# Optimization experiments

Measured on AMD Instinct MI355X. Metric: run time of the kernel, lower is better.

## Reference

```python
import jax, jax.numpy as jnp
import numpy as np

H = 4096      # hidden_size
NH = 32       # num heads
HD = H // NH  # head_dim = 128
I = 11008     # intermediate_size
T = 2048      # num tokens (single prompt sequence)
G = 128       # AWQ group size
EPS = 1e-6
ROPE_BASE = 10000.0


def _make_qlinear(key, k_in, n_out):
    k1, k2, k3 = jax.random.split(key, 3)
    qw = jax.random.randint(k1, (k_in, n_out), 0, 16, dtype=jnp.int32)
    qz = jax.random.randint(k2, (k_in // G, n_out), 0, 16, dtype=jnp.int32)
    scales = jax.random.uniform(k3, (k_in // G, n_out), dtype=jnp.float32) * 0.01 + 1e-3
    return qw, scales, qz


def setup_inputs() -> dict:
    key = jax.random.key(0)
    ks = jax.random.split(key, 8)
    inp = {
        "positions": jnp.arange(T, dtype=jnp.int64),
        "hidden_states": jax.random.normal(ks[0], (T, H), dtype=jnp.float32),
        "input_ln_w": jnp.ones((H,), dtype=jnp.float32),
        "post_ln_w": jnp.ones((H,), dtype=jnp.float32),
    }
    inp["qkv_qw"], inp["qkv_scales"], inp["qkv_qz"] = _make_qlinear(ks[1], H, 3 * H)
    inp["o_qw"], inp["o_scales"], inp["o_qz"] = _make_qlinear(ks[2], H, H)
    inp["gu_qw"], inp["gu_scales"], inp["gu_qz"] = _make_qlinear(ks[3], H, 2 * I)
    inp["down_qw"], inp["down_scales"], inp["down_qz"] = _make_qlinear(ks[4], I, H)
    return inp


def rms_norm(x, w):
    var = jnp.mean(x * x, axis=-1, keepdims=True)
    return x * jax.lax.rsqrt(var + EPS) * w


def awq_linear(x, qw, scales, qz):
    # dequant: (q - z) * scale, group-wise along K; then dense GEMM
    w = (qw.astype(scales.dtype) - jnp.repeat(qz.astype(scales.dtype), G, axis=0)) \
        * jnp.repeat(scales, G, axis=0)
    return x @ w


def apply_rope(x, positions):
    # x: [T, NH, HD], neox-style half rotation, rotary_dim = HD
    inv_freq = 1.0 / (ROPE_BASE ** (jnp.arange(0, HD, 2, dtype=jnp.float32) / HD))
    ang = positions.astype(jnp.float32)[:, None] * inv_freq  # [T, HD/2]
    cos = jnp.cos(ang)[:, None, :]
    sin = jnp.sin(ang)[:, None, :]
    x1, x2 = x[..., : HD // 2], x[..., HD // 2:]
    return jnp.concatenate([x1 * cos - x2 * sin, x2 * cos + x1 * sin], axis=-1)


def reference(positions, hidden_states, input_ln_w, post_ln_w,
              qkv_qw, qkv_scales, qkv_qz, o_qw, o_scales, o_qz,
              gu_qw, gu_scales, gu_qz, down_qw, down_scales, down_qz):
    residual = hidden_states
    x = rms_norm(hidden_states, input_ln_w)

    # attention
    qkv = awq_linear(x, qkv_qw, qkv_scales, qkv_qz)  # [T, 3H]
    q, k, v = jnp.split(qkv, 3, axis=-1)
    q = apply_rope(q.reshape(T, NH, HD), positions)
    k = apply_rope(k.reshape(T, NH, HD), positions)
    v = v.reshape(T, NH, HD)
    scale = HD ** -0.5
    scores = jnp.einsum('qhd,khd->hqk', q, k) * scale  # [NH, T, T]
    causal = jnp.tril(jnp.ones((T, T), dtype=bool))
    scores = jnp.where(causal[None], scores, jnp.finfo(scores.dtype).min)
    probs = jax.nn.softmax(scores, axis=-1)
    attn = jnp.einsum('hqk,khd->qhd', probs, v).reshape(T, H)
    attn_out = awq_linear(attn, o_qw, o_scales, o_qz)

    hidden = residual + attn_out
    residual = hidden
    x = rms_norm(hidden, post_ln_w)

    # MLP: gate_up -> silu(gate) * up -> down
    gate_up = awq_linear(x, gu_qw, gu_scales, gu_qz)  # [T, 2I]
    gate, up = jnp.split(gate_up, 2, axis=-1)
    x = jax.nn.silu(gate) * up
    x = awq_linear(x, down_qw, down_scales, down_qz)
    return residual + x
```

## Files before the change

### kernel.cpp

```cpp
#include <hip/hip_runtime.h>
#include <stdint.h>

#define T_SEQ 2048
#define HID 4096
#define NHEADS 32
#define I_FF 11008
#define QKV_N 12288
#define GU_N 22016

typedef unsigned short u16;
typedef unsigned int u32;
typedef __attribute__((ext_vector_type(4))) float f32x4;
typedef __attribute__((ext_vector_type(8))) __bf16 bf16x8;
typedef __attribute__((ext_vector_type(4))) u32 u32x4;
typedef __attribute__((ext_vector_type(2))) u32 u32x2;

__device__ __forceinline__ u16 f2bf(float f) {
  union { float f; u32 u; } v; v.f = f;
  u32 u = v.u;
  return (u16)((u + 0x7fffu + ((u >> 16) & 1u)) >> 16);
}
__device__ __forceinline__ float bf2f(u16 h) {
  union { u32 u; float f; } v; v.u = ((u32)h) << 16;
  return v.f;
}
__device__ __forceinline__ void split2(float x, u16& hi, u16& lo) {
  hi = f2bf(x);
  lo = f2bf(x - bf2f(hi));
}
__device__ __forceinline__ void split8(const float* v, u32x4& H, u32x4& L) {
#pragma unroll
  for (int j = 0; j < 4; j++) {
    u16 h0, l0, h1, l1;
    split2(v[2 * j], h0, l0);
    split2(v[2 * j + 1], h1, l1);
    H[j] = (u32)h0 | ((u32)h1 << 16);
    L[j] = (u32)l0 | ((u32)l1 << 16);
  }
}
__device__ __forceinline__ void dq8(u32 rbp, int zq, u32x4& w) {
#pragma unroll
  for (int j = 0; j < 4; j++) {
    int q0 = (int)((rbp >> (8 * j)) & 15u) - zq;
    int q1 = (int)((rbp >> (8 * j + 4)) & 15u) - zq;
    u32 b0 = __builtin_bit_cast(u32, (float)q0);
    u32 b1 = __builtin_bit_cast(u32, (float)q1);
    w[j] = (b0 >> 16) | (b1 & 0xffff0000u);
  }
}

__global__ __launch_bounds__(256) void pack_qw_kernel(
    const int* __restrict__ qw, u32* __restrict__ pw, int N) {
  int n = blockIdx.x * 256 + threadIdx.x;
  int oct = blockIdx.y;
  const int* src = qw + (size_t)oct * 8 * N + n;
  u32 v = 0;
#pragma unroll
  for (int j = 0; j < 8; j++)
    v |= ((u32)src[(size_t)j * N] & 15u) << (4 * j);
  pw[(size_t)oct * N + n] = v;
}

__global__ __launch_bounds__(256) void rmsnorm_kernel(
    const float* __restrict__ in, const float* __restrict__ w,
    u16* __restrict__ outh, u16* __restrict__ outl) {
  int row = blockIdx.x;
  const float* x = in + (size_t)row * HID;
  float4 vals[4];
  float ss = 0.f;
#pragma unroll
  for (int k = 0; k < 4; k++) {
    vals[k] = ((const float4*)x)[threadIdx.x + k * 256];
    ss += vals[k].x * vals[k].x + vals[k].y * vals[k].y +
          vals[k].z * vals[k].z + vals[k].w * vals[k].w;
  }
#pragma unroll
  for (int o = 1; o < 64; o <<= 1) ss += __shfl_xor(ss, o);
  __shared__ float red[4];
  if ((threadIdx.x & 63) == 0) red[threadIdx.x >> 6] = ss;
  __syncthreads();
  ss = red[0] + red[1] + red[2] + red[3];
  float rs = rsqrtf(ss * (1.f / HID) + 1e-6f);
#pragma unroll
  for (int k = 0; k < 4; k++) {
    int c4 = threadIdx.x + k * 256;
    float4 wv = ((const float4*)w)[c4];
    float o[4] = {vals[k].x * rs * wv.x, vals[k].y * rs * wv.y,
                  vals[k].z * rs * wv.z, vals[k].w * rs * wv.w};
    u32x2 H, L;
#pragma unroll
    for (int j = 0; j < 2; j++) {
      u16 h0, l0, h1, l1;
      split2(o[2 * j], h0, l0);
      split2(o[2 * j + 1], h1, l1);
      H[j] = (u32)h0 | ((u32)h1 << 16);
      L[j] = (u32)l0 | ((u32)l1 << 16);
    }
    *(u32x2*)(outh + (size_t)row * HID + c4 * 4) = H;
    *(u32x2*)(outl + (size_t)row * HID + c4 * 4) = L;
  }
}

template <bool RESID, bool OUTBF16>
__global__ __launch_bounds__(512) void awq_gemm_kernel(
    const u16* __restrict__ Ahg, const u16* __restrict__ Alg,
    const u32* __restrict__ pw, const float* __restrict__ scales,
    const int* __restrict__ qz, const float* __restrict__ resid,
    void* __restrict__ outp, int N, int K, int nstrips) {
  __shared__ u16 AhL[2][128][40];
  __shared__ u16 AlL[2][128][40];
  __shared__ u16 BqL[2][128][40];
  int tid = threadIdx.x;
  int lane = tid & 63;
  int wid = tid >> 6;
  int g16 = lane >> 4, l16 = lane & 15;
  int p = blockIdx.x;
  int xcd = p & 7;
  int idx = p >> 3;
  int s = idx >> 1;
  int mi = ((idx & 1) << 3) + xcd;
  if (s >= nstrips) return;
  int m0 = mi * 128;
  int n0 = s * 128;
  int wr = wid >> 1, wc = wid & 1;

  f32x4 acc[2][4] = {};
  float svold[4];

  int a_row = tid >> 2, a_kc = (tid & 3) * 8;
  const u16* aph = Ahg + (size_t)(m0 + a_row) * K + a_kc;
  const u16* apl = Alg + (size_t)(m0 + a_row) * K + a_kc;
  int b_n = tid & 127, b_kb = (tid >> 7) * 8;
  const u32* pwp = pw + (size_t)(tid >> 7) * N + n0 + b_n;
  const float* scp = scales + n0;
  const int* qzp = qz + n0 + b_n;

  int nsteps = K >> 5;

  u32x4 rah, ral;
  u32 rbp;

  auto load_step = [&](int ks) {
    int k0 = ks << 5;
    rah = *(const u32x4*)(aph + k0);
    ral = *(const u32x4*)(apl + k0);
    rbp = pwp[(size_t)(ks << 2) * N];
  };
  auto write_step = [&](int buf, int zq) {
    *(u32x4*)&AhL[buf][a_row][a_kc] = rah;
    *(u32x4*)&AlL[buf][a_row][a_kc] = ral;
    u32x4 w;
    dq8(rbp, zq, w);
    *(u32x4*)&BqL[buf][b_n][b_kb] = w;
  };

  int zq = qzp[0];
  load_step(0);
  write_step(0, zq);
#pragma unroll
  for (int n = 0; n < 4; n++)
    svold[n] = scp[wc * 64 + n * 16 + l16];
  __syncthreads();

  int cur = 0;
  for (int ks = 0; ks < nsteps; ks++) {
    int nxt = ks + 1;
    if (nxt < nsteps) {
      if ((nxt & 3) == 0) zq = qzp[(size_t)(nxt >> 2) * N];
      load_step(nxt);
    }
    if (ks != 0 && (ks & 3) == 0) {
      int g = ks >> 2;
#pragma unroll
      for (int n = 0; n < 4; n++) {
        float svnew = scp[(size_t)g * N + wc * 64 + n * 16 + l16];
        float r = svold[n] * __builtin_amdgcn_rcpf(svnew);
        svold[n] = svnew;
#pragma unroll
        for (int m = 0; m < 2; m++)
#pragma unroll
          for (int i = 0; i < 4; i++) acc[m][n][i] *= r;
      }
    }
    bf16x8 bq[4];
#pragma unroll
    for (int n = 0; n < 4; n++)
      bq[n] = __builtin_bit_cast(bf16x8,
          *(const u32x4*)&BqL[cur][wc * 64 + n * 16 + l16][g16 * 8]);
#pragma unroll
    for (int m = 0; m < 2; m++) {
      bf16x8 ah = __builtin_bit_cast(bf16x8,
          *(const u32x4*)&AhL[cur][wr * 32 + m * 16 + l16][g16 * 8]);
      bf16x8 al = __builtin_bit_cast(bf16x8,
          *(const u32x4*)&AlL[cur][wr * 32 + m * 16 + l16][g16 * 8]);
#pragma unroll
      for (int n = 0; n < 4; n++) {
        acc[m][n] = __builtin_amdgcn_mfma_f32_16x16x32_bf16(al, bq[n], acc[m][n], 0, 0, 0);
        acc[m][n] = __builtin_amdgcn_mfma_f32_16x16x32_bf16(ah, bq[n], acc[m][n], 0, 0, 0);
      }
    }
    if (nxt < nsteps) write_step(cur ^ 1, zq);
    __syncthreads();
    cur ^= 1;
  }
#pragma unroll
  for (int n = 0; n < 4; n++)
#pragma unroll
    for (int m = 0; m < 2; m++)
#pragma unroll
      for (int i = 0; i < 4; i++) acc[m][n][i] *= svold[n];
#pragma unroll
  for (int m = 0; m < 2; m++) {
#pragma unroll
    for (int n = 0; n < 4; n++) {
#pragma unroll
      for (int r = 0; r < 4; r++) {
        int row = m0 + wr * 32 + m * 16 + g16 * 4 + r;
        int col = n0 + wc * 64 + n * 16 + l16;
        float v = acc[m][n][r];
        if (RESID) v += resid[(size_t)row * N + col];
        if (OUTBF16)
          ((u16*)outp)[(size_t)row * N + col] = f2bf(v);
        else
          ((float*)outp)[(size_t)row * N + col] = v;
      }
    }
  }
}

template <bool RESID, bool OUTBF16>
__global__ __launch_bounds__(512) void awq_gemm256_kernel(
    const u16* __restrict__ Ahg,
    const u32* __restrict__ pw, const float* __restrict__ scales,
    const int* __restrict__ qz, const float* __restrict__ resid,
    void* __restrict__ outp, int N, int K, int nstrips) {
  __shared__ u16 AhL[2][128][40];
  __shared__ u16 BqL[2][256][40];
  int tid = threadIdx.x;
  int lane = tid & 63;
  int wid = tid >> 6;
  int g16 = lane >> 4, l16 = lane & 15;
  int p = blockIdx.x;
  int xcd = p & 7;
  int idx = p >> 3;
  int s = idx >> 1;
  int mi = ((idx & 1) << 3) + xcd;
  if (s >= nstrips) return;
  int m0 = mi * 128;
  int n0 = s * 256;
  int wr = wid >> 2, wc = wid & 3;

  f32x4 acc[4][4] = {};
  float svold[4];

  int a_row = tid >> 2, a_kc = (tid & 3) * 8;
  const u16* aph = Ahg + (size_t)(m0 + a_row) * K + a_kc;
  int b_n = tid & 255;
  int b_oct = (tid >> 8) * 2;
  int b_kb = b_oct * 8;
  const u32* pwp = pw + (size_t)b_oct * N + n0 + b_n;
  const float* scp = scales + n0;
  const int* qzp = qz + n0 + b_n;

  int nsteps = K >> 5;

  u32x4 rah;
  u32 rb0, rb1;

  auto load_step = [&](int ks) {
    int k0 = ks << 5;
    rah = *(const u32x4*)(aph + k0);
    const u32* q = pwp + (size_t)(ks << 2) * N;
    rb0 = q[0];
    rb1 = q[N];
  };
  auto write_step = [&](int buf, int zq) {
    *(u32x4*)&AhL[buf][a_row][a_kc] = rah;
    u32x4 w0, w1;
    dq8(rb0, zq, w0);
    dq8(rb1, zq, w1);
    *(u32x4*)&BqL[buf][b_n][b_kb] = w0;
    *(u32x4*)&BqL[buf][b_n][b_kb + 8] = w1;
  };

  int zq = qzp[0];
  load_step(0);
  write_step(0, zq);
#pragma unroll
  for (int n = 0; n < 4; n++)
    svold[n] = scp[wc * 64 + n * 16 + l16];
  __syncthreads();

  int cur = 0;
  for (int ks = 0; ks < nsteps; ks++) {
    int nxt = ks + 1;
    if (nxt < nsteps) {
      if ((nxt & 3) == 0) zq = qzp[(size_t)(nxt >> 2) * N];
      load_step(nxt);
    }
    if (ks != 0 && (ks & 3) == 0) {
      int g = ks >> 2;
#pragma unroll
      for (int n = 0; n < 4; n++) {
        float svnew = scp[(size_t)g * N + wc * 64 + n * 16 + l16];
        float r = svold[n] * __builtin_amdgcn_rcpf(svnew);
        svold[n] = svnew;
#pragma unroll
        for (int m = 0; m < 4; m++)
#pragma unroll
          for (int i = 0; i < 4; i++) acc[m][n][i] *= r;
      }
    }
    bf16x8 bq[4];
#pragma unroll
    for (int n = 0; n < 4; n++)
      bq[n] = __builtin_bit_cast(bf16x8,
          *(const u32x4*)&BqL[cur][wc * 64 + n * 16 + l16][g16 * 8]);
#pragma unroll
    for (int m = 0; m < 4; m++) {
      bf16x8 ah = __builtin_bit_cast(bf16x8,
          *(const u32x4*)&AhL[cur][wr * 64 + m * 16 + l16][g16 * 8]);
#pragma unroll
      for (int n = 0; n < 4; n++)
        acc[m][n] = __builtin_amdgcn_mfma_f32_16x16x32_bf16(ah, bq[n], acc[m][n], 0, 0, 0);
    }
    if (nxt < nsteps) write_step(cur ^ 1, zq);
    __syncthreads();
    cur ^= 1;
  }
#pragma unroll
  for (int n = 0; n < 4; n++)
#pragma unroll
    for (int m = 0; m < 4; m++)
#pragma unroll
      for (int i = 0; i < 4; i++) acc[m][n][i] *= svold[n];
#pragma unroll
  for (int m = 0; m < 4; m++) {
#pragma unroll
    for (int n = 0; n < 4; n++) {
#pragma unroll
      for (int r = 0; r < 4; r++) {
        int row = m0 + wr * 64 + m * 16 + g16 * 4 + r;
        int col = n0 + wc * 64 + n * 16 + l16;
        float v = acc[m][n][r];
        if (RESID) v += resid[(size_t)row * N + col];
        if (OUTBF16)
          ((u16*)outp)[(size_t)row * N + col] = f2bf(v);
        else
          ((float*)outp)[(size_t)row * N + col] = v;
      }
    }
  }
}

__global__ __launch_bounds__(256) void rope_kernel(float* __restrict__ qkv) {
  int t = blockIdx.x;
  __shared__ float cs[64], sn[64];
  if (threadIdx.x < 64) {
    int i = threadIdx.x;
    float freq = exp2f(-(float)i * (13.287712379549449f / 64.f));
    float ang = (float)t * freq;
    cs[i] = cosf(ang);
    sn[i] = sinf(ang);
  }
  __syncthreads();
#pragma unroll
  for (int it = 0; it < 16; it++) {
    int idx = threadIdx.x + it * 256;
    int part = idx >> 11;
    int rem = idx & 2047;
    int hh = rem >> 6, i = rem & 63;
    float* base = qkv + (size_t)t * QKV_N + (size_t)part * HID + hh * 128;
    float x1 = base[i], x2 = base[64 + i];
    float c = cs[i], s = sn[i];
    base[i] = x1 * c - x2 * s;
    base[64 + i] = x2 * c + x1 * s;
  }
}

__global__ __launch_bounds__(256) void transpose_v_kernel(
    const float* __restrict__ qkv, u16* __restrict__ vt) {
  __shared__ u16 tile[64][65];
  int tb = blockIdx.x;
  int cb = blockIdx.y;
  int tid = threadIdx.x;
  int r = tid >> 2, c16 = (tid & 3) * 16;
  const float* src = qkv + (size_t)(tb * 64 + r) * QKV_N + 2 * HID + cb * 64 + c16;
  float v[16];
  *(float4*)&v[0] = *(const float4*)(src);
  *(float4*)&v[4] = *(const float4*)(src + 4);
  *(float4*)&v[8] = *(const float4*)(src + 8);
  *(float4*)&v[12] = *(const float4*)(src + 12);
#pragma unroll
  for (int i = 0; i < 16; i++) tile[r][c16 + i] = f2bf(v[i]);
  __syncthreads();
  int ocol = tid >> 2, tchunk = (tid & 3) * 16;
  u16 vbuf[16];
#pragma unroll
  for (int i = 0; i < 16; i++) vbuf[i] = tile[tchunk + i][ocol];
  u16* dst = vt + (size_t)(cb * 64 + ocol) * T_SEQ + tb * 64 + tchunk;
  *(u32x4*)dst = *(u32x4*)&vbuf[0];
  *(u32x4*)(dst + 8) = *(u32x4*)&vbuf[8];
}

__global__ __launch_bounds__(256) void attn_kernel(
    const float* __restrict__ qkv, const u16* __restrict__ vt,
    u16* __restrict__ outh, u16* __restrict__ outl) {
  constexpr float SCALE = 0.08838834764831845f;
  __shared__ u16 Kh[32][136], Kl[32][136];
  __shared__ u16 Vt_lds[128][40];
  __shared__ u16 P_lds[4][16][40];
  int tid = threadIdx.x;
  int wid = tid >> 6, lane = tid & 63;
  int g16 = lane >> 4, l16 = lane & 15;
  int h = blockIdx.x & 31;
  int qt = blockIdx.x >> 5;
  int qb = qt * 64;

  bf16x8 qh[4], ql[4];
  {
    const float* qsrc = qkv + (size_t)(qb + wid * 16 + l16) * QKV_N + h * 128;
#pragma unroll
    for (int ds = 0; ds < 4; ds++) {
      float v[8];
      *(float4*)&v[0] = *(const float4*)(qsrc + ds * 32 + g16 * 8);
      *(float4*)&v[4] = *(const float4*)(qsrc + ds * 32 + g16 * 8 + 4);
      u32x4 H, L;
      split8(v, H, L);
      qh[ds] = __builtin_bit_cast(bf16x8, H);
      ql[ds] = __builtin_bit_cast(bf16x8, L);
    }
  }
  f32x4 oacc[8] = {};
  float mrun[4] = {-1e30f, -1e30f, -1e30f, -1e30f};
  float lrun[4] = {0.f, 0.f, 0.f, 0.f};

  int st_k = tid >> 3, st_d = (tid & 7) * 16;
  int sv_d = tid >> 1, sv_k = (tid & 1) * 16;

  int ktiles = (qb + 64) >> 5;
  for (int kt = 0; kt < ktiles; kt++) {
    __syncthreads();
    {
      const float* src = qkv + (size_t)(kt * 32 + st_k) * QKV_N + HID + h * 128 + st_d;
      float v[16];
      *(float4*)&v[0] = *(const float4*)(src);
      *(float4*)&v[4] = *(const float4*)(src + 4);
      *(float4*)&v[8] = *(const float4*)(src + 8);
      *(float4*)&v[12] = *(const float4*)(src + 12);
      u32x4 H, L;
      split8(&v[0], H, L);
      *(u32x4*)&Kh[st_k][st_d] = H;
      *(u32x4*)&Kl[st_k][st_d] = L;
      split8(&v[8], H, L);
      *(u32x4*)&Kh[st_k][st_d + 8] = H;
      *(u32x4*)&Kl[st_k][st_d + 8] = L;
    }
    {
      const u16* src = vt + (size_t)(h * 128 + sv_d) * T_SEQ + kt * 32 + sv_k;
      *(u32x4*)&Vt_lds[sv_d][sv_k] = *(const u32x4*)src;
      *(u32x4*)&Vt_lds[sv_d][sv_k + 8] = *(const u32x4*)(src + 8);
    }
    __syncthreads();
    f32x4 sacc[2] = {};
#pragma unroll
    for (int kb = 0; kb < 2; kb++)
#pragma unroll
      for (int ds = 0; ds < 4; ds++) {
        bf16x8 kfh = __builtin_bit_cast(bf16x8,
            *(const u32x4*)&Kh[kb * 16 + l16][ds * 32 + g16 * 8]);
        bf16x8 kfl = __builtin_bit_cast(bf16x8,
            *(const u32x4*)&Kl[kb * 16 + l16][ds * 32 + g16 * 8]);
        sacc[kb] = __builtin_amdgcn_mfma_f32_16x16x32_bf16(qh[ds], kfh, sacc[kb], 0, 0, 0);
        sacc[kb] = __builtin_amdgcn_mfma_f32_16x16x32_bf16(ql[ds], kfh, sacc[kb], 0, 0, 0);
        sacc[kb] = __builtin_amdgcn_mfma_f32_16x16x32_bf16(qh[ds], kfl, sacc[kb], 0, 0, 0);
      }
    float p0v[4], p1v[4];
#pragma unroll
    for (int r = 0; r < 4; r++) {
      int qrow = qb + wid * 16 + g16 * 4 + r;
      bool msk0 = (kt * 32 + l16) > qrow;
      bool msk1 = (kt * 32 + 16 + l16) > qrow;
      float s0 = msk0 ? -1e30f : sacc[0][r] * SCALE;
      float s1 = msk1 ? -1e30f : sacc[1][r] * SCALE;
      float tm = fmaxf(s0, s1);
      tm = fmaxf(tm, __shfl_xor(tm, 1));
      tm = fmaxf(tm, __shfl_xor(tm, 2));
      tm = fmaxf(tm, __shfl_xor(tm, 4));
      tm = fmaxf(tm, __shfl_xor(tm, 8));
      float mnew = fmaxf(mrun[r], tm);
      float fac = __expf(mrun[r] - mnew);
      float p0 = msk0 ? 0.f : __expf(s0 - mnew);
      float p1 = msk1 ? 0.f : __expf(s1 - mnew);
      float ts = p0 + p1;
      ts += __shfl_xor(ts, 1);
      ts += __shfl_xor(ts, 2);
      ts += __shfl_xor(ts, 4);
      ts += __shfl_xor(ts, 8);
      lrun[r] = lrun[r] * fac + ts;
      mrun[r] = mnew;
      p0v[r] = p0; p1v[r] = p1;
#pragma unroll
      for (int db = 0; db < 8; db++) oacc[db][r] *= fac;
    }
#pragma unroll
    for (int r = 0; r < 4; r++) {
      P_lds[wid][g16 * 4 + r][l16] = f2bf(p0v[r]);
      P_lds[wid][g16 * 4 + r][16 + l16] = f2bf(p1v[r]);
    }
    __syncthreads();
    bf16x8 pa = __builtin_bit_cast(bf16x8, *(const u32x4*)&P_lds[wid][l16][g16 * 8]);
#pragma unroll
    for (int db = 0; db < 8; db++) {
      bf16x8 vb = __builtin_bit_cast(bf16x8,
          *(const u32x4*)&Vt_lds[db * 16 + l16][g16 * 8]);
      oacc[db] = __builtin_amdgcn_mfma_f32_16x16x32_bf16(pa, vb, oacc[db], 0, 0, 0);
    }
  }
#pragma unroll
  for (int r = 0; r < 4; r++) {
    int qrow = qb + wid * 16 + g16 * 4 + r;
    float inv = 1.f / lrun[r];
#pragma unroll
    for (int db = 0; db < 8; db++) {
      float v = oacc[db][r] * inv;
      u16 h16, l16v;
      split2(v, h16, l16v);
      size_t idx = (size_t)qrow * HID + h * 128 + db * 16 + l16;
      outh[idx] = h16;
      outl[idx] = l16v;
    }
  }
}

__global__ __launch_bounds__(256) void silu_mul_kernel(
    const u16* __restrict__ gu, u16* __restrict__ acth) {
  size_t e = ((size_t)blockIdx.x * 256 + threadIdx.x) * 8;
  size_t row = e / I_FF;
  int col = (int)(e % I_FF);
  const u16* gp = gu + row * GU_N + col;
  u32x4 gv = *(const u32x4*)gp;
  u32x4 uv = *(const u32x4*)(gp + I_FF);
  u32x4 H;
#pragma unroll
  for (int j = 0; j < 4; j++) {
    float g0 = bf2f((u16)(gv[j] & 0xffff)), g1 = bf2f((u16)(gv[j] >> 16));
    float u0 = bf2f((u16)(uv[j] & 0xffff)), u1 = bf2f((u16)(uv[j] >> 16));
    float o0 = g0 / (1.f + __expf(-g0)) * u0;
    float o1 = g1 / (1.f + __expf(-g1)) * u1;
    H[j] = (u32)f2bf(o0) | ((u32)f2bf(o1) << 16);
  }
  *(u32x4*)(acth + row * I_FF + col) = H;
}

extern "C" void kernel_launch(void* const* d_in, const int* in_sizes, int n_in,
                              void* d_out, int out_size, void* d_ws, size_t ws_size,
                              hipStream_t stream) {
  const float* hs    = (const float*)d_in[1];
  const float* ln1   = (const float*)d_in[2];
  const float* ln2   = (const float*)d_in[3];
  const int* qkv_qw  = (const int*)d_in[4];
  const float* qkv_s = (const float*)d_in[5];
  const int* qkv_z   = (const int*)d_in[6];
  const int* o_qw    = (const int*)d_in[7];
  const float* o_s   = (const float*)d_in[8];
  const int* o_z     = (const int*)d_in[9];
  const int* gu_qw   = (const int*)d_in[10];
  const float* gu_s  = (const float*)d_in[11];
  const int* gu_z    = (const int*)d_in[12];
  const int* dn_qw   = (const int*)d_in[13];
  const float* dn_s  = (const float*)d_in[14];
  const int* dn_z    = (const int*)d_in[15];

  char* ws = (char*)d_ws;
  u16*   xnh    = (u16*)(ws);
  u16*   xnl    = (u16*)(ws + (size_t)16777216);
  float* qkv    = (float*)(ws + (size_t)33554432);
  u16*   vt     = (u16*)(ws + (size_t)134217728);
  float* hidden = (float*)(ws + (size_t)150994944);
  u16*   gup    = (u16*)(ws + (size_t)184549376);
  u16*   attnh  = xnh;
  u16*   attnl  = xnl;
  u16*   acth   = (u16*)qkv;
  u32* pk_gup = (u32*)gup;
  u32* pk_qkv = (u32*)((char*)qkv + (size_t)50331648);

  auto grid128 = [](int N) { return 16 * (N / 128); };
  auto grid256 = [](int N) { return 16 * (N / 256); };

  rmsnorm_kernel<<<T_SEQ, 256, 0, stream>>>(hs, ln1, xnh, xnl);
  pack_qw_kernel<<<dim3(QKV_N / 256, HID / 8), 256, 0, stream>>>(qkv_qw, pk_gup, QKV_N);
  awq_gemm_kernel<false, false><<<grid128(QKV_N), 512, 0, stream>>>(
      xnh, xnl, pk_gup, qkv_s, qkv_z, nullptr, qkv, QKV_N, HID, QKV_N / 128);
  rope_kernel<<<T_SEQ, 256, 0, stream>>>(qkv);
  transpose_v_kernel<<<dim3(T_SEQ / 64, HID / 64), 256, 0, stream>>>(qkv, vt);
  attn_kernel<<<NHEADS * (T_SEQ / 64), 256, 0, stream>>>(qkv, vt, attnh, attnl);
  pack_qw_kernel<<<dim3(HID / 256, HID / 8), 256, 0, stream>>>(o_qw, pk_gup, HID);
  awq_gemm256_kernel<true, false><<<grid256(HID), 512, 0, stream>>>(
      attnh, pk_gup, o_s, o_z, hs, hidden, HID, HID, HID / 256);
  rmsnorm_kernel<<<T_SEQ, 256, 0, stream>>>(hidden, ln2, xnh, xnl);
  pack_qw_kernel<<<dim3(GU_N / 256, HID / 8), 256, 0, stream>>>(gu_qw, pk_qkv, GU_N);
  awq_gemm256_kernel<false, true><<<grid256(GU_N), 512, 0, stream>>>(
      xnh, pk_qkv, gu_s, gu_z, nullptr, gup, GU_N, HID, GU_N / 256);
  silu_mul_kernel<<<(T_SEQ * (size_t)I_FF / 8 / 256), 256, 0, stream>>>(gup, acth);
  pack_qw_kernel<<<dim3(HID / 256, I_FF / 8), 256, 0, stream>>>(dn_qw, pk_gup, HID);
  awq_gemm256_kernel<true, false><<<grid256(HID), 512, 0, stream>>>(
      acth, pk_gup, dn_s, dn_z, hidden, (float*)d_out, HID, I_FF, HID / 256);
}
```

Measured before the change: 1.804 ms.

## Pre-dequantize AWQ weights to N-major bf16 before the 256-wide GEMMs

Adds a pack kernel that subtracts zero points and converts the int4 weights to bf16, stored N-major with K contiguous. The o-proj, gate/up and down GEMMs then copy bf16 tiles straight into LDS with 16-byte loads instead of unpacking nibbles and dequantizing in the inner loop. Gate/up is split into two half launches so the bf16 weight buffer fits in the workspace. The trade is about four times more weight bytes written and read through global memory, in exchange for less ALU work and simpler shared-memory staging inside the GEMM.

```diff
diff --git a/kernel.cpp b/kernel.cpp
--- a/kernel.cpp
+++ b/kernel.cpp
@@ -59,6 +59,27 @@
   for (int j = 0; j < 8; j++)
     v |= ((u32)src[(size_t)j * N] & 15u) << (4 * j);
   pw[(size_t)oct * N + n] = v;
+}
+
+__global__ __launch_bounds__(256) void pack_dqb_kernel(
+    const int* __restrict__ qw, const int* __restrict__ qz,
+    u16* __restrict__ bw, int N, int K, int n_base) {
+  int nl = blockIdx.x * 256 + threadIdx.x;
+  int n = n_base + nl;
+  int k0 = blockIdx.y * 32;
+  int zq = qz[(size_t)(k0 >> 7) * N + n];
+  u16 row[32];
+#pragma unroll
+  for (int j = 0; j < 32; j++) {
+    int q = qw[(size_t)(k0 + j) * N + n];
+    u32 b = __builtin_bit_cast(u32, (float)(q - zq));
+    row[j] = (u16)(b >> 16);
+  }
+  u16* dst = bw + (size_t)nl * K + k0;
+  *(u32x4*)dst = *(u32x4*)&row[0];
+  *(u32x4*)(dst + 8) = *(u32x4*)&row[8];
+  *(u32x4*)(dst + 16) = *(u32x4*)&row[16];
+  *(u32x4*)(dst + 24) = *(u32x4*)&row[24];
 }
 
 __global__ __launch_bounds__(256) void rmsnorm_kernel(
@@ -229,11 +250,10 @@
 }
 
 template <bool RESID, bool OUTBF16>
-__global__ __launch_bounds__(512) void awq_gemm256_kernel(
-    const u16* __restrict__ Ahg,
-    const u32* __restrict__ pw, const float* __restrict__ scales,
-    const int* __restrict__ qz, const float* __restrict__ resid,
-    void* __restrict__ outp, int N, int K, int nstrips) {
+__global__ __launch_bounds__(512) void awq_gemm256b_kernel(
+    const u16* __restrict__ Ahg, const u16* __restrict__ bw,
+    const float* __restrict__ scales, const float* __restrict__ resid,
+    void* __restrict__ outp, int N, int K, int nstrips, int n_base) {
   __shared__ u16 AhL[2][128][40];
   __shared__ u16 BqL[2][256][40];
   int tid = threadIdx.x;
@@ -247,7 +267,8 @@
   int mi = ((idx & 1) << 3) + xcd;
   if (s >= nstrips) return;
   int m0 = mi * 128;
-  int n0 = s * 256;
+  int n0l = s * 256;
+  int n0 = n_base + n0l;
   int wr = wid >> 2, wc = wid & 3;
 
   f32x4 acc[4][4] = {};
@@ -255,37 +276,28 @@
 
   int a_row = tid >> 2, a_kc = (tid & 3) * 8;
   const u16* aph = Ahg + (size_t)(m0 + a_row) * K + a_kc;
-  int b_n = tid & 255;
-  int b_oct = (tid >> 8) * 2;
-  int b_kb = b_oct * 8;
-  const u32* pwp = pw + (size_t)b_oct * N + n0 + b_n;
+  int b_row = tid >> 1, b_kc = (tid & 1) * 16;
+  const u16* bwp = bw + (size_t)(n0l + b_row) * K + b_kc;
   const float* scp = scales + n0;
-  const int* qzp = qz + n0 + b_n;
 
   int nsteps = K >> 5;
 
-  u32x4 rah;
-  u32 rb0, rb1;
+  u32x4 rah, rb0, rb1;
 
   auto load_step = [&](int ks) {
     int k0 = ks << 5;
     rah = *(const u32x4*)(aph + k0);
-    const u32* q = pwp + (size_t)(ks << 2) * N;
-    rb0 = q[0];
-    rb1 = q[N];
+    rb0 = *(const u32x4*)(bwp + k0);
+    rb1 = *(const u32x4*)(bwp + k0 + 8);
   };
-  auto write_step = [&](int buf, int zq) {
+  auto write_step = [&](int buf) {
     *(u32x4*)&AhL[buf][a_row][a_kc] = rah;
-    u32x4 w0, w1;
-    dq8(rb0, zq, w0);
-    dq8(rb1, zq, w1);
-    *(u32x4*)&BqL[buf][b_n][b_kb] = w0;
-    *(u32x4*)&BqL[buf][b_n][b_kb + 8] = w1;
+    *(u32x4*)&BqL[buf][b_row][b_kc] = rb0;
+    *(u32x4*)&BqL[buf][b_row][b_kc + 8] = rb1;
   };
 
-  int zq = qzp[0];
   load_step(0);
-  write_step(0, zq);
+  write_step(0);
 #pragma unroll
   for (int n = 0; n < 4; n++)
     svold[n] = scp[wc * 64 + n * 16 + l16];
@@ -294,10 +306,7 @@
   int cur = 0;
   for (int ks = 0; ks < nsteps; ks++) {
     int nxt = ks + 1;
-    if (nxt < nsteps) {
-      if ((nxt & 3) == 0) zq = qzp[(size_t)(nxt >> 2) * N];
-      load_step(nxt);
-    }
+    if (nxt < nsteps) load_step(nxt);
     if (ks != 0 && (ks & 3) == 0) {
       int g = ks >> 2;
 #pragma unroll
@@ -324,7 +333,7 @@
       for (int n = 0; n < 4; n++)
         acc[m][n] = __builtin_amdgcn_mfma_f32_16x16x32_bf16(ah, bq[n], acc[m][n], 0, 0, 0);
     }
-    if (nxt < nsteps) write_step(cur ^ 1, zq);
+    if (nxt < nsteps) write_step(cur ^ 1);
     __syncthreads();
     cur ^= 1;
   }
@@ -582,28 +591,41 @@
   u16*   attnh  = xnh;
   u16*   attnl  = xnl;
   u16*   acth   = (u16*)qkv;
-  u32* pk_gup = (u32*)gup;
-  u32* pk_qkv = (u32*)((char*)qkv + (size_t)50331648);
+  u32* pk_nib  = (u32*)gup;
+  u16* bw_gup  = (u16*)gup;
+  u16* bw_qkv  = (u16*)qkv;
 
   auto grid128 = [](int N) { return 16 * (N / 128); };
-  auto grid256 = [](int N) { return 16 * (N / 256); };
+  auto grid256 = [](int ncols) { return 16 * (ncols / 256); };
 
   rmsnorm_kernel<<<T_SEQ, 256, 0, stream>>>(hs, ln1, xnh, xnl);
-  pack_qw_kernel<<<dim3(QKV_N / 256, HID / 8), 256, 0, stream>>>(qkv_qw, pk_gup, QKV_N);
+  pack_qw_kernel<<<dim3(QKV_N / 256, HID / 8), 256, 0, stream>>>(qkv_qw, pk_nib, QKV_N);
   awq_gemm_kernel<false, false><<<grid128(QKV_N), 512, 0, stream>>>(
-      xnh, xnl, pk_gup, qkv_s, qkv_z, nullptr, qkv, QKV_N, HID, QKV_N / 128);
+      xnh, xnl, pk_nib, qkv_s, qkv_z, nullptr, qkv, QKV_N, HID, QKV_N / 128);
   rope_kernel<<<T_SEQ, 256, 0, stream>>>(qkv);
   transpose_v_kernel<<<dim3(T_SEQ / 64, HID / 64), 256, 0, stream>>>(qkv, vt);
   attn_kernel<<<NHEADS * (T_SEQ / 64), 256, 0, stream>>>(qkv, vt, attnh, attnl);
-  pack_qw_kernel<<<dim3(HID / 256, HID / 8), 256, 0, stream>>>(o_qw, pk_gup, HID);
-  awq_gemm256_kernel<true, false><<<grid256(HID), 512, 0, stream>>>(
-      attnh, pk_gup, o_s, o_z, hs, hidden, HID, HID, HID / 256);
+
+  pack_dqb_kernel<<<dim3(HID / 256, HID / 32), 256, 0, stream>>>(
+      o_qw, o_z, bw_gup, HID, HID, 0);
+  awq_gemm256b_kernel<true, false><<<grid256(HID), 512, 0, stream>>>(
+      attnh, bw_gup, o_s, hs, hidden, HID, HID, HID / 256, 0);
+
   rmsnorm_kernel<<<T_SEQ, 256, 0, stream>>>(hidden, ln2, xnh, xnl);
-  pack_qw_kernel<<<dim3(GU_N / 256, HID / 8), 256, 0, stream>>>(gu_qw, pk_qkv, GU_N);
-  awq_gemm256_kernel<false, true><<<grid256(GU_N), 512, 0, stream>>>(
-      xnh, pk_qkv, gu_s, gu_z, nullptr, gup, GU_N, HID, GU_N / 256);
+
+  pack_dqb_kernel<<<dim3(I_FF / 256, HID / 32), 256, 0, stream>>>(
+      gu_qw, gu_z, bw_qkv, GU_N, HID, 0);
+  awq_gemm256b_kernel<false, true><<<grid256(I_FF), 512, 0, stream>>>(
+      xnh, bw_qkv, gu_s, nullptr, gup, GU_N, HID, I_FF / 256, 0);
+  pack_dqb_kernel<<<dim3(I_FF / 256, HID / 32), 256, 0, stream>>>(
+      gu_qw, gu_z, bw_qkv, GU_N, HID, I_FF);
+  awq_gemm256b_kernel<false, true><<<grid256(I_FF), 512, 0, stream>>>(
+      xnh, bw_qkv, gu_s, nullptr, gup, GU_N, HID, I_FF / 256, I_FF);
+
   silu_mul_kernel<<<(T_SEQ * (size_t)I_FF / 8 / 256), 256, 0, stream>>>(gup, acth);
-  pack_qw_kernel<<<dim3(HID / 256, I_FF / 8), 256, 0, stream>>>(dn_qw, pk_gup, HID);
-  awq_gemm256_kernel<true, false><<<grid256(HID), 512, 0, stream>>>(
-      acth, pk_gup, dn_s, dn_z, hidden, (float*)d_out, HID, I_FF, HID / 256);
-}
+
+  pack_dqb_kernel<<<dim3(HID / 256, I_FF / 32), 256, 0, stream>>>(
+      dn_qw, dn_z, bw_gup, HID, I_FF, 0);
+  awq_gemm256b_kernel<true, false><<<grid256(HID), 512, 0, stream>>>(
+      acth, bw_gup, dn_s, hidden, (float*)d_out, HID, I_FF, HID / 256, 0);
+}
```

After: 2.024 ms. +12.2%, slower.
